# Kernel tuning notes

Measured on AMD Instinct MI355X. Metric: run time of the kernel, lower is better.

## Reference

```python
import jax, jax.numpy as jnp
import numpy as np
import math

# model dims
B, S, T = 4, 256, 8
D_MODEL, D_STATE, N_HEAD, NUM_LAYERS = 256, 128, 4, 2
VOCAB = 32000
D_HEAD = D_STATE // N_HEAD
# AdaptiveLIFNeuron constants
TAU, BASE_THR, ADAPT, TARGET = 2.0, 1.0, 0.1, 0.02
DECAY = math.exp(-1.0 / TAU)


@jax.custom_vjp
def spike_fn(x):
    # spikingjelly surrogate.ATan forward = heaviside
    return (x >= 0).astype(x.dtype)

def _spike_fwd(x):
    return spike_fn(x), x

def _spike_bwd(x, g):
    # ATan surrogate gradient, alpha=2: 1 / (1 + (pi*x)^2)
    return (g / (1.0 + (math.pi * x) ** 2),)

spike_fn.defvjp(_spike_fwd, _spike_bwd)


def lif_step(x, v, thr):
    v_pot = v * DECAY + x
    spike = spike_fn(v_pot - jax.lax.stop_gradient(thr))
    v_new = v_pot * (1.0 - jax.lax.stop_gradient(spike))  # reset where spiked
    err = jax.lax.stop_gradient(spike.mean() - TARGET)    # torch.no_grad threshold update
    thr_new = jnp.maximum(thr + ADAPT * err, 0.5)
    return spike, v_new, thr_new


def ssm_layer(x_tbsd, A, C, Wq, bq, Wkv, bkv, Wo, bo):
    # x_tbsd: [T, B, S, d_model] spikes/embeddings, scanned over time
    scale = 1.0 / math.sqrt(D_HEAD)

    def step(carry, x_t):
        h, sv, ov, ts, to = carry
        st = h @ A.T                                      # [B,S,d_state]
        q = (h @ Wq.T + bq).reshape(B * S, N_HEAD, D_HEAD)
        kv = x_t @ Wkv.T + bkv                            # [B,S,2*d_state]
        k, v = jnp.split(kv, 2, axis=-1)
        k = k.reshape(B * S, N_HEAD, D_HEAD)
        v = v.reshape(B * S, N_HEAD, D_HEAD)
        # attention across all B*S positions (faithful to torch reshape)
        scores = jnp.einsum('ahd,bhd->hab', q, k) * scale  # [H, BS, BS]
        attn = jax.nn.softmax(scores, axis=-1)
        att = jnp.einsum('hab,bhd->ahd', attn, v).reshape(B, S, D_STATE)
        upd = st + att @ Wo.T + bo
        h2, sv2, ts2 = lif_step(upd, sv, ts)
        out_pot = h2 @ C.T                                 # [B,S,d_model]
        os_, ov2, to2 = lif_step(out_pot, ov, to)
        return (h2, sv2, ov2, ts2, to2), os_

    init = (jnp.zeros((B, S, D_STATE)), jnp.zeros((B, S, D_STATE)),
            jnp.zeros((B, S, D_MODEL)),
            jnp.full((D_STATE,), BASE_THR), jnp.full((D_MODEL,), BASE_THR))
    _, outs = jax.lax.scan(step, init, x_tbsd)
    return outs  # [T,B,S,d_model]


def setup_inputs() -> dict:
    key = jax.random.key(0)
    ks = jax.random.split(key, 8)
    nrm = lambda k, shape, s: jax.random.normal(k, shape, jnp.float32) * s
    L = NUM_LAYERS
    return {
        'input_ids': jax.random.randint(ks[0], (B, S), 0, VOCAB),
        'emb': nrm(ks[1], (VOCAB, D_MODEL), 0.02),
        'A': nrm(ks[2], (L, D_STATE, D_STATE), 1.0 / math.sqrt(D_STATE)),
        'C': nrm(ks[3], (L, D_MODEL, D_STATE), 1.0 / math.sqrt(D_STATE)),
        'Wq': nrm(ks[4], (L, D_STATE, D_STATE), 1.0 / math.sqrt(D_STATE)),
        'bq': jnp.zeros((L, D_STATE)),
        'Wkv': nrm(ks[5], (L, 2 * D_STATE, D_MODEL), 1.0 / math.sqrt(D_MODEL)),
        'bkv': jnp.zeros((L, 2 * D_STATE)),
        'Wo': nrm(ks[6], (L, D_STATE, D_STATE), 1.0 / math.sqrt(D_STATE)),
        'bo': jnp.zeros((L, D_STATE)),
        'Wout': nrm(ks[7], (VOCAB, D_MODEL), 1.0 / math.sqrt(D_MODEL)),
        'bout': jnp.zeros((VOCAB,)),
    }


def reference(input_ids, emb, A, C, Wq, bq, Wkv, bkv, Wo, bo, Wout, bout):
    tok = emb[input_ids]                                   # [B,S,d_model]
    # encoder_type='expand': replicate embedding over time steps
    hidden = jnp.broadcast_to(tok[None], (T, B, S, D_MODEL))
    for l in range(NUM_LAYERS):
        hidden = ssm_layer(hidden, A[l], C[l], Wq[l], bq[l],
                           Wkv[l], bkv[l], Wo[l], bo[l])
    time_integrated = hidden.mean(axis=0)                  # mean over time -> [B,S,d_model]
    logits = time_integrated @ Wout.T + bout               # output_projection -> [B,S,vocab]
    return logits
```

## Files before the change

### kernel.cpp

```cpp
#include <hip/hip_runtime.h>
#include <math.h>

#define BS_TOT   1024
#define DM       256
#define DST      128
#define TSTEPS   8
#define DECAYF   0.6065306597126334f
#define SCALEF   0.17677669529663689f
#define NE       (BS_TOT * DM)

__global__ void embed_k(const int* __restrict__ ids, const float* __restrict__ emb,
                        float* __restrict__ tok) {
    int r = blockIdx.x, c = threadIdx.x;
    tok[r * DM + c] = emb[(size_t)ids[r] * DM + c];
}

__global__ void prep_k(float* __restrict__ h, float* __restrict__ sv, float* __restrict__ ov,
                       float* __restrict__ W1T, float* __restrict__ WoT, float* __restrict__ CT,
                       const float* __restrict__ Al, const float* __restrict__ Wql,
                       const float* __restrict__ Wol, const float* __restrict__ Cl,
                       int* __restrict__ cnts) {
    int i = blockIdx.x * 256 + threadIdx.x;
    if (i < BS_TOT * DST) { h[i] = 0.f; sv[i] = 0.f; }
    ov[i] = 0.f;
    if (i < 32768) {
        int k = i >> 8, n = i & 255;
        W1T[i] = (n < 128) ? Al[n * 128 + k] : Wql[(n - 128) * 128 + k];
        CT[i]  = Cl[n * 128 + k];
    }
    if (i < 16384) {
        int k = i >> 7, n = i & 127;
        WoT[i] = Wol[n * 128 + k];
    }
    if (i < 16) cnts[i] = 0;
}

__global__ __launch_bounds__(256) void ktrans_k(const float* __restrict__ kv,
                                                float* __restrict__ kT) {
    __shared__ float tile[64][133];
    const float* src = kv + (size_t)blockIdx.y * NE;
    float* dst = kT + (size_t)blockIdx.y * (128 * 1024);
    const int kc = blockIdx.x, tid = threadIdx.x;
#pragma unroll
    for (int i = 0; i < 32; ++i) {
        int idx = i * 256 + tid;
        int key = idx >> 7, d = idx & 127;
        tile[key][d] = src[(size_t)(kc * 64 + key) * 256 + d];
    }
    __syncthreads();
#pragma unroll
    for (int i = 0; i < 32; ++i) {
        int idx = i * 256 + tid;
        int d = idx >> 6, key = idx & 63;
        dst[(size_t)d * 1024 + kc * 64 + key] = tile[key][d];
    }
}

__global__ void mean_k(const float* __restrict__ outs, float* __restrict__ ti) {
    int i = blockIdx.x * 256 + threadIdx.x;
    float s = 0.f;
#pragma unroll
    for (int t = 0; t < TSTEPS; ++t) s += outs[t * NE + i];
    ti[i] = s * 0.125f;
}

template <int BM, int BN, int BK, int TM, int TN>
__global__ __launch_bounds__((BM / TM) * (BN / TN))
void gemm_k(const float* __restrict__ Amat, const float* __restrict__ Wmat,
            const float* __restrict__ bias, float* __restrict__ outp,
            int M, int N, int K) {
    constexpr int NT  = (BM / TM) * (BN / TN);
    constexpr int NXT = BN / TN;
    __shared__ float As[BK][BM + 4];
    __shared__ float Bs[BK][BN + 4];
    const int tid = threadIdx.x;
    const int n0 = blockIdx.x * BN, m0 = blockIdx.y * BM;
    const int tx = tid % NXT, ty = tid / NXT;
    float acc[TM][TN] = {};

    for (int k0 = 0; k0 < K; k0 += BK) {
#pragma unroll
        for (int i = 0; i < (BM * BK) / NT; ++i) {
            int idx = i * NT + tid;
            int kk = idx % BK, mm = idx / BK;
            As[kk][mm] = Amat[(size_t)(m0 + mm) * K + k0 + kk];
        }
#pragma unroll
        for (int i = 0; i < (BN * BK) / NT; ++i) {
            int idx = i * NT + tid;
            int kk = idx % BK, nn = idx / BK;
            Bs[kk][nn] = Wmat[(size_t)(n0 + nn) * K + k0 + kk];
        }
        __syncthreads();
#pragma unroll
        for (int kk = 0; kk < BK; ++kk) {
            float a[TM], b[TN];
#pragma unroll
            for (int i = 0; i < TM; ++i) a[i] = As[kk][ty * TM + i];
#pragma unroll
            for (int j = 0; j < TN; ++j) b[j] = Bs[kk][tx * TN + j];
#pragma unroll
            for (int i = 0; i < TM; ++i)
#pragma unroll
                for (int j = 0; j < TN; ++j) acc[i][j] += a[i] * b[j];
        }
        __syncthreads();
    }
#pragma unroll
    for (int i = 0; i < TM; ++i) {
        int mr = m0 + ty * TM + i;
#pragma unroll
        for (int j = 0; j < TN; ++j) {
            int nc = n0 + tx * TN + j;
            float x = acc[i][j];
            if (bias) x += bias[nc];
            outp[(size_t)mr * N + nc] = x;
        }
    }
}

__global__ __launch_bounds__(256) void gemm_out_k(
    const float* __restrict__ Amat, const float* __restrict__ Wmat,
    const float* __restrict__ bias, float* __restrict__ outp)
{
    constexpr int BM = 128, BN = 128, BK = 32;
    constexpr int K = 256, N = 32000;
    __shared__ float As[BK][BM + 4];
    __shared__ float Bs[BK][BN + 4];
    const int tid = threadIdx.x;

    const int bid = blockIdx.x;
    const int g   = (bid & 7) * 250 + (bid >> 3);
    const int m0  = (g & 7) * BM;
    const int n0  = (g >> 3) * BN;

    const int tx = tid & 15, ty = tid >> 4;
    float acc[8][8] = {};

    for (int k0 = 0; k0 < K; k0 += BK) {
#pragma unroll
        for (int i = 0; i < 4; ++i) {
            int idx = i * 256 + tid;
            int mm = idx >> 3, k4 = idx & 7;
            float4 va = *(const float4*)&Amat[(size_t)(m0 + mm) * K + k0 + k4 * 4];
            As[k4 * 4 + 0][mm] = va.x; As[k4 * 4 + 1][mm] = va.y;
            As[k4 * 4 + 2][mm] = va.z; As[k4 * 4 + 3][mm] = va.w;
            float4 vb = *(const float4*)&Wmat[(size_t)(n0 + mm) * K + k0 + k4 * 4];
            Bs[k4 * 4 + 0][mm] = vb.x; Bs[k4 * 4 + 1][mm] = vb.y;
            Bs[k4 * 4 + 2][mm] = vb.z; Bs[k4 * 4 + 3][mm] = vb.w;
        }
        __syncthreads();
#pragma unroll
        for (int kk = 0; kk < BK; ++kk) {
            float a[8], b[8];
            *(float4*)&a[0] = *(const float4*)&As[kk][ty * 4];
            *(float4*)&a[4] = *(const float4*)&As[kk][64 + ty * 4];
            *(float4*)&b[0] = *(const float4*)&Bs[kk][tx * 4];
            *(float4*)&b[4] = *(const float4*)&Bs[kk][64 + tx * 4];
#pragma unroll
            for (int i = 0; i < 8; ++i)
#pragma unroll
                for (int j = 0; j < 8; ++j) acc[i][j] += a[i] * b[j];
        }
        __syncthreads();
    }

    float bv[8];
    *(float4*)&bv[0] = *(const float4*)&bias[n0 + tx * 4];
    *(float4*)&bv[4] = *(const float4*)&bias[n0 + 64 + tx * 4];
#pragma unroll
    for (int i = 0; i < 8; ++i) {
        const int mr = m0 + ((i < 4) ? (ty * 4 + i) : (64 + ty * 4 + i - 4));
        float4 o0, o1;
        o0.x = acc[i][0] + bv[0]; o0.y = acc[i][1] + bv[1];
        o0.z = acc[i][2] + bv[2]; o0.w = acc[i][3] + bv[3];
        o1.x = acc[i][4] + bv[4]; o1.y = acc[i][5] + bv[5];
        o1.z = acc[i][6] + bv[6]; o1.w = acc[i][7] + bv[7];
        float* dst = &outp[(size_t)mr * N + n0];
        *(float4*)(dst + tx * 4)      = o0;
        *(float4*)(dst + 64 + tx * 4) = o1;
    }
}

__global__ __launch_bounds__(256) void lif_k(
    const float* __restrict__ W1T,
    const float* __restrict__ WoT,
    const float* __restrict__ CT,
    const float* __restrict__ bq_w,
    const float* __restrict__ bo_w,
    float* __restrict__ h,
    float* __restrict__ sv,
    float* __restrict__ ov,
    const float* __restrict__ att_in,
    float* __restrict__ outs_prev,
    float* __restrict__ q_g,
    int* __restrict__ cnt1, int* __restrict__ cnt2, int t, int do_B)
{
    __shared__ float hA_s[4 * 128];
    __shared__ float h2_s[4 * 128];
    __shared__ float att_s[4 * 128];
    __shared__ unsigned long long umr_s[4][2];
    __shared__ unsigned long long um_s[2];
    __shared__ float thr_s[2];

    const int tid = threadIdx.x;
    const int r0 = blockIdx.x * 4;

    if (tid == 0) {
        float ts = 1.0f, to = 1.0f;
        for (int i = 0; i < t - 1; ++i) {
            float e1 = (float)cnt1[i] * (1.f / 131072.f) - 0.02f;
            ts = fmaxf(ts + 0.1f * e1, 0.5f);
            float e2 = (float)cnt2[i] * (1.f / 262144.f) - 0.02f;
            to = fmaxf(to + 0.1f * e2, 0.5f);
        }
        thr_s[0] = ts; thr_s[1] = to;
    }
    hA_s[tid]       = h[r0 * 128 + tid];
    hA_s[256 + tid] = h[r0 * 128 + 256 + tid];
    if (t > 0) {
        att_s[tid]       = att_in[r0 * 128 + tid];
        att_s[256 + tid] = att_in[r0 * 128 + 256 + tid];
    }
    __syncthreads();
    {
        int w = tid >> 6, l = tid & 63;
        unsigned long long b0 = __ballot(hA_s[w * 128 + l] != 0.f);
        unsigned long long b1 = __ballot(hA_s[w * 128 + 64 + l] != 0.f);
        if (l == 0) { umr_s[w][0] = b0; umr_s[w][1] = b1; }
    }
    __syncthreads();
    if (tid == 0) {
        um_s[0] = umr_s[0][0] | umr_s[1][0] | umr_s[2][0] | umr_s[3][0];
        um_s[1] = umr_s[0][1] | umr_s[1][1] | umr_s[2][1] | umr_s[3][1];
    }
    __syncthreads();

    const int n = tid & 127, half = tid >> 7;
    const int ra = half * 2, rb = half * 2 + 1;

    if (t > 0) {
        float sta = 0.f, stb = 0.f;
        unsigned long long u = um_s[0];
        while (u) {
            int k = __builtin_ctzll(u); u &= u - 1;
            float w = W1T[(k << 8) + n];
            sta += hA_s[ra * 128 + k] * w; stb += hA_s[rb * 128 + k] * w;
        }
        u = um_s[1];
        while (u) {
            int kk = __builtin_ctzll(u); u &= u - 1;
            int k = 64 + kk;
            float w = W1T[(k << 8) + n];
            sta += hA_s[ra * 128 + k] * w; stb += hA_s[rb * 128 + k] * w;
        }
        float ba = 0.f, bb = 0.f;
        for (int i4 = 0; i4 < 32; ++i4) {
            const int i = i4 * 4;
            float w0 = WoT[(i + 0) * 128 + n];
            float w1 = WoT[(i + 1) * 128 + n];
            float w2 = WoT[(i + 2) * 128 + n];
            float w3 = WoT[(i + 3) * 128 + n];
            float4 aa = *(const float4*)&att_s[ra * 128 + i];
            float4 ab = *(const float4*)&att_s[rb * 128 + i];
            ba += aa.x * w0; ba += aa.y * w1; ba += aa.z * w2; ba += aa.w * w3;
            bb += ab.x * w0; bb += ab.y * w1; bb += ab.z * w2; bb += ab.w * w3;
        }
        float ts = thr_s[0];
        float xa = ba + bo_w[n]; xa += sta;
        float va = sv[(r0 + ra) * 128 + n];
        float vpa = va * DECAYF + xa;
        float spa = (vpa - ts >= 0.f) ? 1.f : 0.f;
        h[(r0 + ra) * 128 + n]  = spa;
        sv[(r0 + ra) * 128 + n] = vpa * (1.f - spa);
        h2_s[ra * 128 + n] = spa;

        float xb = bb + bo_w[n]; xb += stb;
        float vb = sv[(r0 + rb) * 128 + n];
        float vpb = vb * DECAYF + xb;
        float spb = (vpb - ts >= 0.f) ? 1.f : 0.f;
        h[(r0 + rb) * 128 + n]  = spb;
        sv[(r0 + rb) * 128 + n] = vpb * (1.f - spb);
        h2_s[rb * 128 + n] = spb;

        unsigned long long bba = __ballot(spa != 0.f);
        unsigned long long bbb = __ballot(spb != 0.f);
        int w = tid >> 6, l = tid & 63;
        if (l == 0) {
            umr_s[ra][w & 1] = bba;
            umr_s[rb][w & 1] = bbb;
            atomicAdd(&cnt1[t - 1], __popcll(bba) + __popcll(bbb));
        }
    } else {
        h2_s[tid]       = hA_s[tid];
        h2_s[256 + tid] = hA_s[256 + tid];
    }
    __syncthreads();
    if (tid == 0) {
        um_s[0] = umr_s[0][0] | umr_s[1][0] | umr_s[2][0] | umr_s[3][0];
        um_s[1] = umr_s[0][1] | umr_s[1][1] | umr_s[2][1] | umr_s[3][1];
    }
    __syncthreads();

    if (t > 0) {
        const int n2 = tid;
        float a0 = 0.f, a1 = 0.f, a2 = 0.f, a3 = 0.f;
        unsigned long long u = um_s[0];
        while (u) {
            int k = __builtin_ctzll(u); u &= u - 1;
            float w = CT[(k << 8) + n2];
            a0 += h2_s[k] * w;       a1 += h2_s[128 + k] * w;
            a2 += h2_s[256 + k] * w; a3 += h2_s[384 + k] * w;
        }
        u = um_s[1];
        while (u) {
            int kk = __builtin_ctzll(u); u &= u - 1;
            int k = 64 + kk;
            float w = CT[(k << 8) + n2];
            a0 += h2_s[k] * w;       a1 += h2_s[128 + k] * w;
            a2 += h2_s[256 + k] * w; a3 += h2_s[384 + k] * w;
        }
        float to = thr_s[1];
        float accs[4] = {a0, a1, a2, a3};
        float sp[4];
#pragma unroll
        for (int r = 0; r < 4; ++r) {
            float vo = ov[(r0 + r) * 256 + n2];
            float vp = vo * DECAYF + accs[r];
            float s = (vp - to >= 0.f) ? 1.f : 0.f;
            sp[r] = s;
            outs_prev[(size_t)(r0 + r) * 256 + n2] = s;
            ov[(r0 + r) * 256 + n2] = vp * (1.f - s);
        }
        unsigned long long c0 = __ballot(sp[0] != 0.f);
        unsigned long long c1 = __ballot(sp[1] != 0.f);
        unsigned long long c2 = __ballot(sp[2] != 0.f);
        unsigned long long c3 = __ballot(sp[3] != 0.f);
        if ((tid & 63) == 0)
            atomicAdd(&cnt2[t - 1], __popcll(c0) + __popcll(c1) + __popcll(c2) + __popcll(c3));
    }

    if (do_B) {
        float qa = 0.f, qb = 0.f;
        unsigned long long u = um_s[0];
        while (u) {
            int k = __builtin_ctzll(u); u &= u - 1;
            float w = W1T[(k << 8) + 128 + n];
            qa += h2_s[ra * 128 + k] * w; qb += h2_s[rb * 128 + k] * w;
        }
        u = um_s[1];
        while (u) {
            int kk = __builtin_ctzll(u); u &= u - 1;
            int k = 64 + kk;
            float w = W1T[(k << 8) + 128 + n];
            qa += h2_s[ra * 128 + k] * w; qb += h2_s[rb * 128 + k] * w;
        }
        q_g[(r0 + ra) * 128 + n] = qa + bq_w[n];
        q_g[(r0 + rb) * 128 + n] = qb + bq_w[n];
    }
}

__global__ __launch_bounds__(256) void attn_k(
    const float* __restrict__ q_g,
    const float* __restrict__ kT,
    const float* __restrict__ kv,
    float* __restrict__ att_out)
{
    __shared__ float p_s[8][1032];
    __shared__ float v_s[64 * 36];
    __shared__ float q_s[8][32];
    __shared__ float red_s[8 * 33];
    __shared__ float mrow_s[8], linv_s[8];

    const int tid = threadIdx.x;
    const int hh = blockIdx.x >> 7;
    const int r0 = (blockIdx.x & 127) * 8;

    {
        int r = tid >> 5, d = tid & 31;
        q_s[r][d] = q_g[(size_t)(r0 + r) * 128 + hh * 32 + d];
    }
    __syncthreads();

    {
        const int w = tid >> 6, l = tid & 63;
        const int key4 = w * 64 + l;
        const float4* kT4 = (const float4*)(kT + (size_t)hh * 32 * 1024);
        float4 acc[8];
#pragma unroll
        for (int r = 0; r < 8; ++r) acc[r] = make_float4(0.f, 0.f, 0.f, 0.f);
#pragma unroll
        for (int pass = 0; pass < 2; ++pass) {
            const int d0 = pass * 16;
            float4 kreg[16];
#pragma unroll
            for (int i = 0; i < 16; ++i) kreg[i] = kT4[(size_t)(d0 + i) * 256 + key4];
#pragma unroll
            for (int i4 = 0; i4 < 4; ++i4) {
#pragma unroll
                for (int r = 0; r < 8; ++r) {
                    float4 qv = *(const float4*)&q_s[r][d0 + i4 * 4];
                    float4 k0 = kreg[i4 * 4 + 0], k1 = kreg[i4 * 4 + 1];
                    float4 k2 = kreg[i4 * 4 + 2], k3 = kreg[i4 * 4 + 3];
                    acc[r].x += qv.x * k0.x; acc[r].x += qv.y * k1.x;
                    acc[r].x += qv.z * k2.x; acc[r].x += qv.w * k3.x;
                    acc[r].y += qv.x * k0.y; acc[r].y += qv.y * k1.y;
                    acc[r].y += qv.z * k2.y; acc[r].y += qv.w * k3.y;
                    acc[r].z += qv.x * k0.z; acc[r].z += qv.y * k1.z;
                    acc[r].z += qv.z * k2.z; acc[r].z += qv.w * k3.z;
                    acc[r].w += qv.x * k0.w; acc[r].w += qv.y * k1.w;
                    acc[r].w += qv.z * k2.w; acc[r].w += qv.w * k3.w;
                }
            }
        }
#pragma unroll
        for (int r = 0; r < 8; ++r) {
            acc[r].x *= SCALEF; acc[r].y *= SCALEF;
            acc[r].z *= SCALEF; acc[r].w *= SCALEF;
            *(float4*)&p_s[r][key4 * 4] = acc[r];
        }
    }
    __syncthreads();

    {
        const int rh = tid >> 5, lg = tid & 31;
        float mx = -1e30f;
        for (int jj = 0; jj < 32; ++jj) mx = fmaxf(mx, p_s[rh][lg + 32 * jj]);
        red_s[rh * 33 + lg] = mx;
        __syncthreads();
        if (tid < 8) {
            float m = red_s[tid * 33];
            for (int j = 1; j < 32; ++j) m = fmaxf(m, red_s[tid * 33 + j]);
            mrow_s[tid] = m;
        }
        __syncthreads();
        float m = mrow_s[rh];
        float ls = 0.f;
        for (int jj = 0; jj < 32; ++jj) {
            int a = lg + 32 * jj;
            float p = expf(p_s[rh][a] - m);
            p_s[rh][a] = p;
            ls += p;
        }
        red_s[rh * 33 + lg] = ls;
        __syncthreads();
        if (tid < 8) {
            float l = 0.f;
            for (int j = 0; j < 32; ++j) l += red_s[tid * 33 + j];
            linv_s[tid] = 1.0f / l;
        }
    }
    __syncthreads();

    {
        const int w = tid >> 6, l = tid & 63;
        const int r = (w & 1) * 4 + (l >> 4);
        const int dp = l & 15;
        const bool act = (w < 2);
        const float4* kv4 = (const float4*)kv;
        float4 stg0, stg1;
        {
            int i0 = tid, i1 = 256 + tid;
            stg0 = kv4[(size_t)(i0 >> 3) * 64 + 32 + hh * 8 + (i0 & 7)];
            stg1 = kv4[(size_t)(i1 >> 3) * 64 + 32 + hh * 8 + (i1 & 7)];
        }
        float a0 = 0.f, a1 = 0.f;
        for (int c = 0; c < 16; ++c) {
            {
                int i0 = tid, i1 = 256 + tid;
                *(float4*)&v_s[(i0 >> 3) * 36 + (i0 & 7) * 4] = stg0;
                *(float4*)&v_s[(i1 >> 3) * 36 + (i1 & 7) * 4] = stg1;
            }
            if (c < 15) {
                int i0 = tid, i1 = 256 + tid;
                stg0 = kv4[(size_t)((c + 1) * 64 + (i0 >> 3)) * 64 + 32 + hh * 8 + (i0 & 7)];
                stg1 = kv4[(size_t)((c + 1) * 64 + (i1 >> 3)) * 64 + 32 + hh * 8 + (i1 & 7)];
            }
            __syncthreads();
            if (act) {
#pragma unroll 4
                for (int k4 = 0; k4 < 16; ++k4) {
                    const int kb = k4 * 4;
                    float4 p4 = *(const float4*)&p_s[r][c * 64 + kb];
                    float2 v0 = *(const float2*)&v_s[(kb + 0) * 36 + 2 * dp];
                    float2 v1 = *(const float2*)&v_s[(kb + 1) * 36 + 2 * dp];
                    float2 v2 = *(const float2*)&v_s[(kb + 2) * 36 + 2 * dp];
                    float2 v3 = *(const float2*)&v_s[(kb + 3) * 36 + 2 * dp];
                    a0 += p4.x * v0.x; a1 += p4.x * v0.y;
                    a0 += p4.y * v1.x; a1 += p4.y * v1.y;
                    a0 += p4.z * v2.x; a1 += p4.z * v2.y;
                    a0 += p4.w * v3.x; a1 += p4.w * v3.y;
                }
            }
            __syncthreads();
        }
        if (act) {
            float li = linv_s[r];
            *(float2*)&att_out[(size_t)(r0 + r) * 128 + hh * 32 + 2 * dp] =
                make_float2(a0 * li, a1 * li);
        }
    }
}

extern "C" void kernel_launch(void* const* d_in, const int* in_sizes, int n_in,
                              void* d_out, int out_size, void* d_ws, size_t ws_size,
                              hipStream_t stream) {
    (void)in_sizes; (void)n_in; (void)out_size; (void)ws_size;
    const int*   ids  = (const int*)d_in[0];
    const float* emb  = (const float*)d_in[1];
    const float* Aw   = (const float*)d_in[2];
    const float* Cw   = (const float*)d_in[3];
    const float* Wq   = (const float*)d_in[4];
    const float* bq   = (const float*)d_in[5];
    const float* Wkv  = (const float*)d_in[6];
    const float* bkv  = (const float*)d_in[7];
    const float* Wo   = (const float*)d_in[8];
    const float* bo   = (const float*)d_in[9];
    const float* Wout = (const float*)d_in[10];
    const float* bout = (const float*)d_in[11];
    float* out = (float*)d_out;
    float* ws  = (float*)d_ws;

    float* tok  = ws;
    float* bufA = tok  + NE;
    float* bufB = bufA + 8 * NE;
    float* kvb  = bufB + 8 * NE;
    float* kTb  = kvb  + 8 * NE;
    float* attb = kTb  + 8 * 131072;
    float* hbuf = attb + 131072;
    float* svb  = hbuf + 131072;
    float* ovb  = svb  + 131072;
    float* qg   = ovb  + 262144;
    float* ti   = qg   + 131072;
    float* W1T  = ti   + NE;
    float* WoT  = W1T  + 32768;
    float* CT   = WoT  + 16384;
    int*   cnts = (int*)(CT + 32768);

    embed_k<<<dim3(1024), dim3(256), 0, stream>>>(ids, emb, tok);

    for (int l = 0; l < 2; ++l) {
        const float* Al   = Aw  + l * 16384;
        const float* Cl   = Cw  + l * 32768;
        const float* Wql  = Wq  + l * 16384;
        const float* bql  = bq  + l * 128;
        const float* Wkvl = Wkv + l * 65536;
        const float* bkvl = bkv + l * 256;
        const float* Wol  = Wo  + l * 16384;
        const float* bol  = bo  + l * 128;
        const float* xin  = (l == 0) ? tok : bufA;
        float* outs       = (l == 0) ? bufA : bufB;
        const int Mkv     = (l == 0) ? BS_TOT : 8 * BS_TOT;
        const int nt      = (l == 0) ? 1 : 8;

        prep_k<<<dim3(1024), dim3(256), 0, stream>>>(hbuf, svb, ovb, W1T, WoT, CT,
                                                     Al, Wql, Wol, Cl, cnts);

        gemm_k<64, 64, 16, 4, 4><<<dim3(256 / 64, Mkv / 64), dim3(256), 0, stream>>>(
            xin, Wkvl, bkvl, kvb, Mkv, 256, 256);

        ktrans_k<<<dim3(16, nt), dim3(256), 0, stream>>>(kvb, kTb);

        for (int t = 0; t <= TSTEPS; ++t) {
            const int do_B = (t < TSTEPS) ? 1 : 0;
            float* outs_prev = outs + (size_t)((t > 0) ? (t - 1) : 0) * NE;
            lif_k<<<dim3(256), dim3(256), 0, stream>>>(
                W1T, WoT, CT, bql, bol,
                hbuf, svb, ovb, attb, outs_prev, qg,
                cnts, cnts + 8, t, do_B);
            if (do_B) {
                const float* kT_t = (l == 0) ? kTb : kTb + (size_t)t * 131072;
                const float* kv_t = (l == 0) ? kvb : kvb + (size_t)t * NE;
                attn_k<<<dim3(512), dim3(256), 0, stream>>>(qg, kT_t, kv_t, attb);
            }
        }
    }

    mean_k<<<dim3(1024), dim3(256), 0, stream>>>(bufB, ti);

    gemm_out_k<<<dim3(2000), dim3(256), 0, stream>>>(ti, Wout, bout, out);
}
```

Measured before the change: 1.241 ms.

## Use per-row spike masks and two rows per block in LIF kernel

Restructures the LIF step kernel so each block handles two rows instead of four, with one 128-thread half per row, and launches 512 blocks. Each row builds its own spike bitmask, so the sparse matvecs skip only that row's zero entries instead of the union across four rows. Because the state is binary, it replaces multiplies with plain adds of weight columns and drops the shared h buffers and one barrier. The cost is less weight reuse across rows per block, meaning more global/L2 weight reads per row.

```diff
diff --git a/kernel.cpp b/kernel.cpp
--- a/kernel.cpp
+++ b/kernel.cpp
@@ -196,15 +196,16 @@
     float* __restrict__ q_g,
     int* __restrict__ cnt1, int* __restrict__ cnt2, int t, int do_B)
 {
-    __shared__ float hA_s[4 * 128];
-    __shared__ float h2_s[4 * 128];
-    __shared__ float att_s[4 * 128];
-    __shared__ unsigned long long umr_s[4][2];
-    __shared__ unsigned long long um_s[2];
+    __shared__ float att_s[2 * 128];
+    __shared__ unsigned long long um1_s[2][2];
+    __shared__ unsigned long long um2_s[2][2];
     __shared__ float thr_s[2];
 
     const int tid = threadIdx.x;
-    const int r0 = blockIdx.x * 4;
+    const int n   = tid & 127;
+    const int hh  = tid >> 7;
+    const int row = blockIdx.x * 2 + hh;
+    const int wh  = (tid >> 6) & 1;
 
     if (tid == 0) {
         float ts = 1.0f, to = 1.0f;
@@ -216,147 +217,88 @@
         }
         thr_s[0] = ts; thr_s[1] = to;
     }
-    hA_s[tid]       = h[r0 * 128 + tid];
-    hA_s[256 + tid] = h[r0 * 128 + 256 + tid];
+
+    const float hval = h[row * 128 + n];
+    if (t > 0) att_s[hh * 128 + n] = att_in[row * 128 + n];
+    {
+        unsigned long long b = __ballot(hval != 0.f);
+        if ((tid & 63) == 0) um1_s[hh][wh] = b;
+    }
+    __syncthreads();
+
+    float sp;
     if (t > 0) {
-        att_s[tid]       = att_in[r0 * 128 + tid];
-        att_s[256 + tid] = att_in[r0 * 128 + 256 + tid];
-    }
-    __syncthreads();
-    {
-        int w = tid >> 6, l = tid & 63;
-        unsigned long long b0 = __ballot(hA_s[w * 128 + l] != 0.f);
-        unsigned long long b1 = __ballot(hA_s[w * 128 + 64 + l] != 0.f);
-        if (l == 0) { umr_s[w][0] = b0; umr_s[w][1] = b1; }
-    }
-    __syncthreads();
-    if (tid == 0) {
-        um_s[0] = umr_s[0][0] | umr_s[1][0] | umr_s[2][0] | umr_s[3][0];
-        um_s[1] = umr_s[0][1] | umr_s[1][1] | umr_s[2][1] | umr_s[3][1];
-    }
-    __syncthreads();
-
-    const int n = tid & 127, half = tid >> 7;
-    const int ra = half * 2, rb = half * 2 + 1;
-
-    if (t > 0) {
-        float sta = 0.f, stb = 0.f;
-        unsigned long long u = um_s[0];
-        while (u) {
-            int k = __builtin_ctzll(u); u &= u - 1;
-            float w = W1T[(k << 8) + n];
-            sta += hA_s[ra * 128 + k] * w; stb += hA_s[rb * 128 + k] * w;
-        }
-        u = um_s[1];
-        while (u) {
-            int kk = __builtin_ctzll(u); u &= u - 1;
-            int k = 64 + kk;
-            float w = W1T[(k << 8) + n];
-            sta += hA_s[ra * 128 + k] * w; stb += hA_s[rb * 128 + k] * w;
-        }
-        float ba = 0.f, bb = 0.f;
+        float st = 0.f;
+        unsigned long long u = um1_s[hh][0];
+        while (u) { int k = __builtin_ctzll(u); u &= u - 1; st += W1T[(k << 8) + n]; }
+        u = um1_s[hh][1];
+        while (u) { int kk = __builtin_ctzll(u); u &= u - 1; st += W1T[((64 + kk) << 8) + n]; }
+        float ba = 0.f;
         for (int i4 = 0; i4 < 32; ++i4) {
             const int i = i4 * 4;
             float w0 = WoT[(i + 0) * 128 + n];
             float w1 = WoT[(i + 1) * 128 + n];
             float w2 = WoT[(i + 2) * 128 + n];
             float w3 = WoT[(i + 3) * 128 + n];
-            float4 aa = *(const float4*)&att_s[ra * 128 + i];
-            float4 ab = *(const float4*)&att_s[rb * 128 + i];
+            float4 aa = *(const float4*)&att_s[hh * 128 + i];
             ba += aa.x * w0; ba += aa.y * w1; ba += aa.z * w2; ba += aa.w * w3;
-            bb += ab.x * w0; bb += ab.y * w1; bb += ab.z * w2; bb += ab.w * w3;
         }
         float ts = thr_s[0];
-        float xa = ba + bo_w[n]; xa += sta;
-        float va = sv[(r0 + ra) * 128 + n];
+        float xa = ba + bo_w[n]; xa += st;
+        float va = sv[row * 128 + n];
         float vpa = va * DECAYF + xa;
-        float spa = (vpa - ts >= 0.f) ? 1.f : 0.f;
-        h[(r0 + ra) * 128 + n]  = spa;
-        sv[(r0 + ra) * 128 + n] = vpa * (1.f - spa);
-        h2_s[ra * 128 + n] = spa;
-
-        float xb = bb + bo_w[n]; xb += stb;
-        float vb = sv[(r0 + rb) * 128 + n];
-        float vpb = vb * DECAYF + xb;
-        float spb = (vpb - ts >= 0.f) ? 1.f : 0.f;
-        h[(r0 + rb) * 128 + n]  = spb;
-        sv[(r0 + rb) * 128 + n] = vpb * (1.f - spb);
-        h2_s[rb * 128 + n] = spb;
-
-        unsigned long long bba = __ballot(spa != 0.f);
-        unsigned long long bbb = __ballot(spb != 0.f);
-        int w = tid >> 6, l = tid & 63;
-        if (l == 0) {
-            umr_s[ra][w & 1] = bba;
-            umr_s[rb][w & 1] = bbb;
-            atomicAdd(&cnt1[t - 1], __popcll(bba) + __popcll(bbb));
-        }
+        sp = (vpa - ts >= 0.f) ? 1.f : 0.f;
+        h[row * 128 + n]  = sp;
+        sv[row * 128 + n] = vpa * (1.f - sp);
     } else {
-        h2_s[tid]       = hA_s[tid];
-        h2_s[256 + tid] = hA_s[256 + tid];
+        sp = hval;
+    }
+    {
+        unsigned long long b = __ballot(sp != 0.f);
+        if ((tid & 63) == 0) {
+            um2_s[hh][wh] = b;
+            if (t > 0) atomicAdd(&cnt1[t - 1], __popcll(b));
+        }
     }
     __syncthreads();
-    if (tid == 0) {
-        um_s[0] = umr_s[0][0] | umr_s[1][0] | umr_s[2][0] | umr_s[3][0];
-        um_s[1] = umr_s[0][1] | umr_s[1][1] | umr_s[2][1] | umr_s[3][1];
-    }
-    __syncthreads();
 
     if (t > 0) {
-        const int n2 = tid;
-        float a0 = 0.f, a1 = 0.f, a2 = 0.f, a3 = 0.f;
-        unsigned long long u = um_s[0];
+        float a0 = 0.f, a1 = 0.f;
+        unsigned long long u = um2_s[hh][0];
         while (u) {
             int k = __builtin_ctzll(u); u &= u - 1;
-            float w = CT[(k << 8) + n2];
-            a0 += h2_s[k] * w;       a1 += h2_s[128 + k] * w;
-            a2 += h2_s[256 + k] * w; a3 += h2_s[384 + k] * w;
-        }
-        u = um_s[1];
+            a0 += CT[(k << 8) + n]; a1 += CT[(k << 8) + 128 + n];
+        }
+        u = um2_s[hh][1];
         while (u) {
             int kk = __builtin_ctzll(u); u &= u - 1;
             int k = 64 + kk;
-            float w = CT[(k << 8) + n2];
-            a0 += h2_s[k] * w;       a1 += h2_s[128 + k] * w;
-            a2 += h2_s[256 + k] * w; a3 += h2_s[384 + k] * w;
+            a0 += CT[(k << 8) + n]; a1 += CT[(k << 8) + 128 + n];
         }
         float to = thr_s[1];
-        float accs[4] = {a0, a1, a2, a3};
-        float sp[4];
-#pragma unroll
-        for (int r = 0; r < 4; ++r) {
-            float vo = ov[(r0 + r) * 256 + n2];
-            float vp = vo * DECAYF + accs[r];
-            float s = (vp - to >= 0.f) ? 1.f : 0.f;
-            sp[r] = s;
-            outs_prev[(size_t)(r0 + r) * 256 + n2] = s;
-            ov[(r0 + r) * 256 + n2] = vp * (1.f - s);
-        }
-        unsigned long long c0 = __ballot(sp[0] != 0.f);
-        unsigned long long c1 = __ballot(sp[1] != 0.f);
-        unsigned long long c2 = __ballot(sp[2] != 0.f);
-        unsigned long long c3 = __ballot(sp[3] != 0.f);
+        float vo0 = ov[row * 256 + n];
+        float vp0 = vo0 * DECAYF + a0;
+        float s0 = (vp0 - to >= 0.f) ? 1.f : 0.f;
+        outs_prev[(size_t)row * 256 + n] = s0;
+        ov[row * 256 + n] = vp0 * (1.f - s0);
+        float vo1 = ov[row * 256 + 128 + n];
+        float vp1 = vo1 * DECAYF + a1;
+        float s1 = (vp1 - to >= 0.f) ? 1.f : 0.f;
+        outs_prev[(size_t)row * 256 + 128 + n] = s1;
+        ov[row * 256 + 128 + n] = vp1 * (1.f - s1);
+        unsigned long long c0 = __ballot(s0 != 0.f);
+        unsigned long long c1 = __ballot(s1 != 0.f);
         if ((tid & 63) == 0)
-            atomicAdd(&cnt2[t - 1], __popcll(c0) + __popcll(c1) + __popcll(c2) + __popcll(c3));
+            atomicAdd(&cnt2[t - 1], __popcll(c0) + __popcll(c1));
     }
 
     if (do_B) {
-        float qa = 0.f, qb = 0.f;
-        unsigned long long u = um_s[0];
-        while (u) {
-            int k = __builtin_ctzll(u); u &= u - 1;
-            float w = W1T[(k << 8) + 128 + n];
-            qa += h2_s[ra * 128 + k] * w; qb += h2_s[rb * 128 + k] * w;
-        }
-        u = um_s[1];
-        while (u) {
-            int kk = __builtin_ctzll(u); u &= u - 1;
-            int k = 64 + kk;
-            float w = W1T[(k << 8) + 128 + n];
-            qa += h2_s[ra * 128 + k] * w; qb += h2_s[rb * 128 + k] * w;
-        }
-        q_g[(r0 + ra) * 128 + n] = qa + bq_w[n];
-        q_g[(r0 + rb) * 128 + n] = qb + bq_w[n];
+        float qa = 0.f;
+        unsigned long long u = um2_s[hh][0];
+        while (u) { int k = __builtin_ctzll(u); u &= u - 1; qa += W1T[(k << 8) + 128 + n]; }
+        u = um2_s[hh][1];
+        while (u) { int kk = __builtin_ctzll(u); u &= u - 1; qa += W1T[((64 + kk) << 8) + 128 + n]; }
+        q_g[row * 128 + n] = qa + bq_w[n];
     }
 }
 
@@ -564,7 +506,7 @@
         for (int t = 0; t <= TSTEPS; ++t) {
             const int do_B = (t < TSTEPS) ? 1 : 0;
             float* outs_prev = outs + (size_t)((t > 0) ? (t - 1) : 0) * NE;
-            lif_k<<<dim3(256), dim3(256), 0, stream>>>(
+            lif_k<<<dim3(512), dim3(256), 0, stream>>>(
                 W1T, WoT, CT, bql, bol,
                 hbuf, svb, ovb, attb, outs_prev, qg,
                 cnts, cnts + 8, t, do_B);
```

After: 1.602 ms. 29.1% more time.
